# Optimization experiments

Measured on AMD Instinct MI355X. Metric: run time of the kernel, lower is better.

## Reference

```python
import jax, jax.numpy as jnp
import numpy as np

N = 50000
E = 800000
IN = 128
HID = 320
HEADS = 4
D = HID // HEADS  # 80
EPS = 1e-5
NEG_SLOPE = 0.2


def sage_conv(x, src, dst, wl, bl, wr, n):
    # PyG SAGEConv (mean aggr): out = lin_l(mean_j x_j) + lin_r(x_i)
    msg = x[src]                                               # [E, HID]
    s = jax.ops.segment_sum(msg, dst, num_segments=n)          # [N, HID]
    cnt = jax.ops.segment_sum(jnp.ones((src.shape[0], 1), x.dtype), dst, num_segments=n)
    mean = s / jnp.maximum(cnt, 1.0)
    return mean @ wl + bl + x @ wr


def gat_conv(x, src, dst, w, a_src, a_dst, b, n):
    # PyG GATConv with add_self_loops=True, concat=True
    loop = jnp.arange(n, dtype=src.dtype)
    src = jnp.concatenate([src, loop])
    dst = jnp.concatenate([dst, loop])
    xh = (x @ w).reshape(n, HEADS, D)                          # [N, H, D]
    al = jnp.sum(xh * a_src, axis=-1)                          # [N, H] (source term)
    ar = jnp.sum(xh * a_dst, axis=-1)                          # [N, H] (target term)
    e = jax.nn.leaky_relu(al[src] + ar[dst], NEG_SLOPE)        # [E', H]
    m = jax.ops.segment_max(e, dst, num_segments=n)            # [N, H]
    m = jnp.where(jnp.isfinite(m), m, 0.0)
    ex = jnp.exp(e - m[dst])                                   # [E', H]
    den = jax.ops.segment_sum(ex, dst, num_segments=n)         # [N, H]
    num = jax.ops.segment_sum(ex[:, :, None] * xh[src], dst, num_segments=n)  # [N, H, D]
    out = num / jnp.maximum(den, 1e-16)[:, :, None]
    return out.reshape(n, HEADS * D) + b


def batch_norm(x, gamma, beta):
    # eval-mode BN with running_mean=0, running_var=1
    return x * (gamma / jnp.sqrt(1.0 + EPS)) + beta


def setup_inputs() -> dict:
    key = jax.random.key(0)
    ks = jax.random.split(key, 24)
    s = 0.05
    inp = {
        'x': jax.random.normal(ks[0], (N, IN), jnp.float32),
        'edge_index': jax.random.randint(ks[1], (2, E), 0, N, jnp.int32),
        'w_in': jax.random.normal(ks[2], (IN, HID), jnp.float32) * s,
        'b_in': jnp.zeros((HID,), jnp.float32),
        'sage0_wl': jax.random.normal(ks[3], (HID, HID), jnp.float32) * s,
        'sage0_bl': jnp.zeros((HID,), jnp.float32),
        'sage0_wr': jax.random.normal(ks[4], (HID, HID), jnp.float32) * s,
        'gat1_w': jax.random.normal(ks[5], (HID, HID), jnp.float32) * s,
        'gat1_asrc': jax.random.normal(ks[6], (HEADS, D), jnp.float32) * s,
        'gat1_adst': jax.random.normal(ks[7], (HEADS, D), jnp.float32) * s,
        'gat1_b': jnp.zeros((HID,), jnp.float32),
        'sage2_wl': jax.random.normal(ks[8], (HID, HID), jnp.float32) * s,
        'sage2_bl': jnp.zeros((HID,), jnp.float32),
        'sage2_wr': jax.random.normal(ks[9], (HID, HID), jnp.float32) * s,
        'gat3_w': jax.random.normal(ks[10], (HID, HID), jnp.float32) * s,
        'gat3_asrc': jax.random.normal(ks[11], (HEADS, D), jnp.float32) * s,
        'gat3_adst': jax.random.normal(ks[12], (HEADS, D), jnp.float32) * s,
        'gat3_b': jnp.zeros((HID,), jnp.float32),
        'bn_gamma': jnp.ones((4, HID), jnp.float32),
        'bn_beta': jnp.zeros((4, HID), jnp.float32),
        'cls_w1': jax.random.normal(ks[13], (HID, HID // 2), jnp.float32) * s,
        'cls_b1': jnp.zeros((HID // 2,), jnp.float32),
        'cls_w2': jax.random.normal(ks[14], (HID // 2, 2), jnp.float32) * s,
        'cls_b2': jnp.zeros((2,), jnp.float32),
    }
    return inp


def reference(x, edge_index, w_in, b_in,
              sage0_wl, sage0_bl, sage0_wr,
              gat1_w, gat1_asrc, gat1_adst, gat1_b,
              sage2_wl, sage2_bl, sage2_wr,
              gat3_w, gat3_asrc, gat3_adst, gat3_b,
              bn_gamma, bn_beta,
              cls_w1, cls_b1, cls_w2, cls_b2):
    src, dst = edge_index[0], edge_index[1]
    h = jax.nn.relu(x @ w_in + b_in)  # dropout is identity in eval
    # layer 0: SAGE
    h = sage_conv(h, src, dst, sage0_wl, sage0_bl, sage0_wr, N)
    h = jax.nn.relu(batch_norm(h, bn_gamma[0], bn_beta[0]))
    # layer 1: GAT
    h = gat_conv(h, src, dst, gat1_w, gat1_asrc, gat1_adst, gat1_b, N)
    h = jax.nn.relu(batch_norm(h, bn_gamma[1], bn_beta[1]))
    # layer 2: SAGE
    h = sage_conv(h, src, dst, sage2_wl, sage2_bl, sage2_wr, N)
    h = jax.nn.relu(batch_norm(h, bn_gamma[2], bn_beta[2]))
    # layer 3: GAT
    h = gat_conv(h, src, dst, gat3_w, gat3_asrc, gat3_adst, gat3_b, N)
    h = jax.nn.relu(batch_norm(h, bn_gamma[3], bn_beta[3]))
    embeddings = h
    out = jax.nn.relu(h @ cls_w1 + cls_b1) @ cls_w2 + cls_b2
    return (out, embeddings)
```

## Files before the change

kernel.cpp:

```cpp
#include <hip/hip_runtime.h>
#include <cstdint>

#define MN 50000
#define EN 800000
#define HID 320
#define HEADS 4
#define HDIM 80
#define NEG_SLOPE 0.2f

typedef __attribute__((ext_vector_type(4))) float f32x4;
typedef __attribute__((ext_vector_type(8))) short short8v;

__device__ __forceinline__ unsigned short f2bf(float f){
  unsigned u = __float_as_uint(f);
  return (unsigned short)((u + 0x7fffu + ((u >> 16) & 1u)) >> 16);
}
__device__ __forceinline__ float bf2f(unsigned short s){
  return __uint_as_float(((unsigned)s) << 16);
}
__device__ __forceinline__ void gldlds16(const void* g, void* l){
  __builtin_amdgcn_global_load_lds((const __attribute__((address_space(1))) void*)g,
                                   (__attribute__((address_space(3))) void*)l, 16, 0, 0);
}

__global__ void hist_kernel(const int* __restrict__ dst, int* __restrict__ hist, int E) {
  int e = blockIdx.x * 256 + threadIdx.x;
  if (e < E) atomicAdd(&hist[dst[e]], 1);
}

__global__ __launch_bounds__(1024) void scan_kernel(const int* __restrict__ hist,
                                                    int* __restrict__ row_off, int n) {
  __shared__ int part[1024];
  int t = threadIdx.x;
  int chunk = (n + 1023) >> 10;
  int beg = t * chunk, end = beg + chunk;
  if (end > n) end = n;
  if (beg > n) beg = n;
  int s = 0;
  for (int i = beg; i < end; i++) s += hist[i];
  part[t] = s;
  __syncthreads();
  for (int off = 1; off < 1024; off <<= 1) {
    int v = (t >= off) ? part[t - off] : 0;
    __syncthreads();
    if (t >= off) part[t] += v;
    __syncthreads();
  }
  int run = (t > 0) ? part[t - 1] : 0;
  for (int i = beg; i < end; i++) { row_off[i] = run; run += hist[i]; }
  if (t == 0) row_off[n] = part[1023];
}

__global__ void scatter_kernel(const int* __restrict__ src, const int* __restrict__ dst,
                               const int* __restrict__ row_off, int* __restrict__ cur,
                               int* __restrict__ csr_src, int E) {
  int e = blockIdx.x * 256 + threadIdx.x;
  if (e < E) {
    int d = dst[e];
    int p = atomicAdd(&cur[d], 1);
    csr_src[row_off[d] + p] = src[e];
  }
}

__global__ void wprep(const float* __restrict__ W, unsigned short* __restrict__ dst,
                      int K, int Nsz, int total) {
  int idx = blockIdx.x * 256 + threadIdx.x;
  if (idx >= total) return;
  int j = idx & 7;
  int c1 = (idx >> 3) & 3;
  int rest = idx >> 5;
  int col = rest % Nsz;
  int kt = rest / Nsz;
  int chunk = c1 ^ ((col >> 1) & 3);
  int kp = kt * 32 + chunk * 8 + j;
  int seg = kp / K;
  int k = kp - seg * K;
  float v = W[(size_t)k * Nsz + col];
  unsigned short h = f2bf(v);
  unsigned short o = (seg == 2) ? f2bf(v - bf2f(h)) : h;
  dst[(size_t)kt * Nsz * 32 + (size_t)col * 32 + c1 * 8 + j] = o;
}

template<int CW, bool SRCF32, int SEGT, int NPASS, int MODE>
__global__ __launch_bounds__(128 * CW, 4) void mfma_gemm(
    const char* __restrict__ A1, const char* __restrict__ A2,
    const char* __restrict__ Wq,
    const float* __restrict__ bias, const float* __restrict__ gamma,
    const float* __restrict__ beta, void* __restrict__ outp, int M)
{
  static_assert(!SRCF32 || CW == 4, "");
  constexpr int TPB = 128 * CW;
  constexpr int N = CW * 80;
  constexpr int NT = NPASS * 3 * SEGT;
  constexpr int TILEB = N * 64;
  constexpr int AIT = (384 + TPB - 1) / TPB;
  constexpr bool SPLITOUT = (MODE >= 2);
  constexpr bool HASBIAS = (MODE >= 1 && MODE <= 3);
  constexpr bool HASBN = (MODE == 3);
  constexpr bool HASRELU = (MODE >= 1 && MODE <= 3);
  __shared__ __align__(16) char ldsA[2 * 7680];
  __shared__ __align__(16) char ldsB[2 * TILEB];
  const int tid = threadIdx.x;
  const int lane = tid & 63;
  const int w = tid >> 6;
  const int rw = w & 1, cwv = w >> 1;
  const int bm = blockIdx.x * 96;
  const int kc = (lane >> 4) & 3;
  const int l15 = lane & 15;

  int aoff[3], boff[5];
  #pragma unroll
  for (int fr = 0; fr < 3; fr++) aoff[fr] = (rw * 48 + fr * 16 + l15) * 80 + kc * 16;
  #pragma unroll
  for (int cf = 0; cf < 5; cf++) {
    int col = cwv * 80 + cf * 16 + l15;
    boff[cf] = col * 64 + ((kc ^ ((col >> 1) & 3)) << 4);
  }

  f32x4 acc[3][5];
  #pragma unroll
  for (int i = 0; i < 3; i++)
    #pragma unroll
    for (int j = 0; j < 5; j++) { f32x4 z = {0.f, 0.f, 0.f, 0.f}; acc[i][j] = z; }

  f32x4 areg[AIT][2];
  auto issueA = [&](int t) -> bool {
    int pass = 0, tt = t;
    if constexpr (NPASS == 2) { pass = t / (3 * SEGT); tt = t - pass * (3 * SEGT); }
    int seg = tt / SEGT;
    int kk = tt - seg * SEGT;
    const char* __restrict__ base = pass ? A2 : A1;
    #pragma unroll
    for (int it = 0; it < AIT; it++) {
      int s = tid + it * TPB;
      if (s < 384) {
        int row = s >> 2, c = s & 3;
        int r = bm + row; if (r >= M) r = M - 1;
        if constexpr (SRCF32) {
          const char* p = base + (size_t)r * 512 + kk * 128 + c * 32;
          areg[it][0] = *(const f32x4*)p;
          areg[it][1] = *(const f32x4*)(p + 16);
        } else {
          const char* p = base + (size_t)r * 1280 + (seg == 1 ? 640 : 0) + kk * 64 + c * 16;
          areg[it][0] = *(const f32x4*)p;
        }
      }
    }
    return seg == 1;
  };
  auto writeA = [&](int buf, bool lo) {
    #pragma unroll
    for (int it = 0; it < AIT; it++) {
      int s = tid + it * TPB;
      if (s < 384) {
        int row = s >> 2, c = s & 3;
        char* d = &ldsA[buf * 7680 + row * 80 + c * 16];
        if constexpr (SRCF32) {
          short8v v;
          #pragma unroll
          for (int j = 0; j < 8; j++) {
            float f = (j < 4) ? areg[it][0][j] : areg[it][1][j - 4];
            unsigned short h = f2bf(f);
            unsigned short o = lo ? f2bf(f - bf2f(h)) : h;
            v[j] = (short)o;
          }
          *(short8v*)d = v;
        } else {
          f32x4 t4 = areg[it][0];
          *(short8v*)d = *(short8v*)&t4;
        }
      }
    }
  };
  auto issueB = [&](int t, int buf) {
    const char* __restrict__ src = Wq + (size_t)t * TILEB;
    for (int s = tid; s < N * 4; s += TPB)
      gldlds16(src + (size_t)s * 16, &ldsB[buf * TILEB + s * 16]);
  };

  bool plo = issueA(0);
  issueB(0, 0);
  writeA(0, plo);
  __syncthreads();

  for (int t = 0; t < NT; ++t) {
    int curb = t & 1, nxt = curb ^ 1;
    bool lo = false;
    if (t + 1 < NT) { lo = issueA(t + 1); issueB(t + 1, nxt); }
    short8v af0 = *(const short8v*)&ldsA[curb * 7680 + aoff[0]];
    short8v af1 = *(const short8v*)&ldsA[curb * 7680 + aoff[1]];
    short8v af2 = *(const short8v*)&ldsA[curb * 7680 + aoff[2]];
    #pragma unroll
    for (int cf = 0; cf < 5; cf++) {
      short8v bv = *(const short8v*)&ldsB[curb * TILEB + boff[cf]];
      acc[0][cf] = __builtin_amdgcn_mfma_f32_16x16x32_bf16(af0, bv, acc[0][cf], 0, 0, 0);
      acc[1][cf] = __builtin_amdgcn_mfma_f32_16x16x32_bf16(af1, bv, acc[1][cf], 0, 0, 0);
      acc[2][cf] = __builtin_amdgcn_mfma_f32_16x16x32_bf16(af2, bv, acc[2][cf], 0, 0, 0);
    }
    if (t + 1 < NT) writeA(nxt, lo);
    __syncthreads();
  }

  const float bnrs = 0.99999500003749971f;
  #pragma unroll
  for (int fr = 0; fr < 3; fr++) {
    int rbase = bm + rw * 48 + fr * 16 + (lane >> 4) * 4;
    #pragma unroll
    for (int cf = 0; cf < 5; cf++) {
      int col = cwv * 80 + cf * 16 + l15;
      float bi = 0.f, sc = 1.f, be = 0.f;
      if constexpr (HASBIAS) bi = bias[col];
      if constexpr (HASBN) { sc = gamma[col] * bnrs; be = beta[col]; }
      #pragma unroll
      for (int rg = 0; rg < 4; rg++) {
        int r = rbase + rg;
        if (r < M) {
          float v = acc[fr][cf][rg];
          if constexpr (HASBIAS) v += bi;
          if constexpr (HASBN) v = v * sc + be;
          if constexpr (HASRELU) v = v > 0.f ? v : 0.f;
          if constexpr (SPLITOUT) {
            unsigned short h = f2bf(v);
            unsigned short g = f2bf(v - bf2f(h));
            unsigned short* o = (unsigned short*)outp;
            o[(size_t)r * 640 + col] = h;
            o[(size_t)r * 640 + 320 + col] = g;
          } else {
            ((float*)outp)[(size_t)r * N + col] = v;
          }
        }
      }
    }
  }
}

__global__ __launch_bounds__(256) void sage_agg_split(const unsigned* __restrict__ hp,
    const int* __restrict__ row_off, const int* __restrict__ csr_src,
    unsigned* __restrict__ outp, int n) {
  int node = blockIdx.x * 8 + (threadIdx.x >> 5);
  int lane = threadIdx.x & 31;
  if (node >= n) return;
  int beg = row_off[node], end = row_off[node + 1];
  float s0[5] = {0,0,0,0,0}, s1[5] = {0,0,0,0,0};
  for (int e = beg; e < end; e++) {
    const unsigned* row = hp + (size_t)csr_src[e] * 320;
    #pragma unroll
    for (int k = 0; k < 5; k++) {
      unsigned dh = row[lane + 32 * k];
      s0[k] += bf2f((unsigned short)dh);
      s1[k] += bf2f((unsigned short)(dh >> 16));
    }
  }
  int deg = end - beg;
  float inv = 1.0f / (float)(deg > 0 ? deg : 1);
  unsigned* orow = outp + (size_t)node * 320;
  #pragma unroll
  for (int k = 0; k < 5; k++) {
    float v0 = s0[k] * inv;
    float v1 = s1[k] * inv;
    unsigned short h0 = f2bf(v0), h1 = f2bf(v1);
    unsigned short g0 = f2bf(v0 - bf2f(h0)), g1 = f2bf(v1 - bf2f(h1));
    orow[lane + 32 * k] = (unsigned)h0 | ((unsigned)h1 << 16);
    orow[160 + lane + 32 * k] = (unsigned)g0 | ((unsigned)g1 << 16);
  }
}

__global__ void gat_prep(const unsigned short* __restrict__ xs,
    const float* __restrict__ asrc, const float* __restrict__ adst,
    float* __restrict__ al, float* __restrict__ ar, int n) {
  int idx = blockIdx.x * 256 + threadIdx.x;
  if (idx >= n * HEADS) return;
  int node = idx >> 2, hh = idx & 3;
  const unsigned short* hi = xs + (size_t)node * 640 + hh * 80;
  const unsigned short* lo = hi + 320;
  const f32x4* as4 = (const f32x4*)(asrc + hh * HDIM);
  const f32x4* ad4 = (const f32x4*)(adst + hh * HDIM);
  float sl = 0.f, sr = 0.f;
  #pragma unroll
  for (int d8 = 0; d8 < 10; d8++) {
    short8v vh = *(const short8v*)(hi + d8 * 8);
    short8v vl = *(const short8v*)(lo + d8 * 8);
    f32x4 a0 = as4[2 * d8], a1 = as4[2 * d8 + 1];
    f32x4 b0 = ad4[2 * d8], b1 = ad4[2 * d8 + 1];
    #pragma unroll
    for (int j = 0; j < 4; j++) {
      float v = bf2f((unsigned short)vh[j]) + bf2f((unsigned short)vl[j]);
      sl += v * a0[j]; sr += v * b0[j];
    }
    #pragma unroll
    for (int j = 0; j < 4; j++) {
      float v = bf2f((unsigned short)vh[4 + j]) + bf2f((unsigned short)vl[4 + j]);
      sl += v * a1[j]; sr += v * b1[j];
    }
  }
  al[idx] = sl;
  ar[idx] = sr;
}

template<bool F32OUT>
__global__ __launch_bounds__(256) void gat_agg(const unsigned short* __restrict__ hp,
    const int* __restrict__ row_off, const int* __restrict__ csr_src,
    const float* __restrict__ al, const float* __restrict__ ar,
    const float* __restrict__ bias, const float* __restrict__ gamma,
    const float* __restrict__ beta, unsigned short* __restrict__ outS,
    float* __restrict__ outF, int n) {
  int node = (blockIdx.x << 2) + (threadIdx.x >> 6);
  int lane = threadIdx.x & 63;
  if (node >= n) return;
  int beg = row_off[node], end = row_off[node + 1];
  const int hh = lane >> 4;
  const int posb = hh * 80 + (lane & 15);

  float arv[4], sh[4];
  f32x4 a4i = *(const f32x4*)(al + (size_t)node * 4);
  #pragma unroll
  for (int h = 0; h < 4; h++) {
    arv[h] = ar[node * 4 + h];
    float v = a4i[h] + arv[h];
    sh[h] = fmaxf(v, NEG_SLOPE * v);
  }
  float den[4] = {1.f, 1.f, 1.f, 1.f};
  const unsigned short* selfrow = hp + (size_t)node * 640;
  float num[5];
  #pragma unroll
  for (int k = 0; k < 5; k++) {
    int p = posb + 16 * k;
    num[k] = bf2f(selfrow[p]) + bf2f(selfrow[320 + p]);
  }

  for (int e = beg; e < end; e++) {
    int s = __builtin_amdgcn_readfirstlane(csr_src[e]);
    f32x4 a4 = *(const f32x4*)(al + (size_t)s * 4);
    float ex[4];
    #pragma unroll
    for (int h = 0; h < 4; h++) {
      float v = a4[h] + arv[h];
      v = fmaxf(v, NEG_SLOPE * v);
      float r = __expf(v - sh[h]);
      ex[h] = r;
      den[h] += r;
    }
    float exsel = hh < 2 ? (hh == 0 ? ex[0] : ex[1]) : (hh == 2 ? ex[2] : ex[3]);
    const unsigned short* __restrict__ row = hp + (size_t)s * 640;
    #pragma unroll
    for (int k = 0; k < 5; k++) num[k] += exsel * bf2f(row[posb + 16 * k]);
  }

  float dsel = hh < 2 ? (hh == 0 ? den[0] : den[1]) : (hh == 2 ? den[2] : den[3]);
  float dinv = 1.0f / dsel;
  const float bnrs = 0.99999500003749971f;
  #pragma unroll
  for (int k = 0; k < 5; k++) {
    int p = posb + 16 * k;
    float v = num[k] * dinv + bias[p];
    v = v * (gamma[p] * bnrs) + beta[p];
    v = fmaxf(v, 0.f);
    unsigned short h2 = f2bf(v);
    outS[(size_t)node * 640 + p] = h2;
    outS[(size_t)node * 640 + 320 + p] = f2bf(v - bf2f(h2));
    if constexpr (F32OUT) outF[(size_t)node * 320 + p] = v;
  }
}

__global__ void cls2_kernel(const float* __restrict__ tbuf, const float* __restrict__ w2,
                            const float* __restrict__ b2, float* __restrict__ out, int M) {
  int r = blockIdx.x * 256 + threadIdx.x;
  if (r >= M) return;
  const f32x4* row = (const f32x4*)(tbuf + (size_t)r * 160);
  float a0 = b2[0], a1 = b2[1];
  #pragma unroll
  for (int d4 = 0; d4 < 40; d4++) {
    f32x4 v = row[d4];
    #pragma unroll
    for (int j = 0; j < 4; j++) {
      int d = d4 * 4 + j;
      a0 += v[j] * w2[2 * d];
      a1 += v[j] * w2[2 * d + 1];
    }
  }
  out[2 * r] = a0;
  out[2 * r + 1] = a1;
}

extern "C" void kernel_launch(void* const* d_in, const int* in_sizes, int n_in,
                              void* d_out, int out_size, void* d_ws, size_t ws_size,
                              hipStream_t stream) {
  const float* x    = (const float*)d_in[0];
  const int*   ei   = (const int*)d_in[1];
  const float* w_in = (const float*)d_in[2];
  const float* b_in = (const float*)d_in[3];
  const float* s0wl = (const float*)d_in[4];
  const float* s0bl = (const float*)d_in[5];
  const float* s0wr = (const float*)d_in[6];
  const float* g1w  = (const float*)d_in[7];
  const float* g1as = (const float*)d_in[8];
  const float* g1ad = (const float*)d_in[9];
  const float* g1b  = (const float*)d_in[10];
  const float* s2wl = (const float*)d_in[11];
  const float* s2bl = (const float*)d_in[12];
  const float* s2wr = (const float*)d_in[13];
  const float* g3w  = (const float*)d_in[14];
  const float* g3as = (const float*)d_in[15];
  const float* g3ad = (const float*)d_in[16];
  const float* g3b  = (const float*)d_in[17];
  const float* bng  = (const float*)d_in[18];
  const float* bnb  = (const float*)d_in[19];
  const float* cw1  = (const float*)d_in[20];
  const float* cb1  = (const float*)d_in[21];
  const float* cw2  = (const float*)d_in[22];
  const float* cb2  = (const float*)d_in[23];

  char* ws = (char*)d_ws;
  size_t off = 0;
  auto alloc = [&](size_t b) {
    void* p = (void*)(ws + off);
    off += (b + 255) & ~(size_t)255;
    return p;
  };
  const size_t SB = (size_t)MN * 1280;
  char* S0 = (char*)alloc(SB);
  char* S1 = (char*)alloc(SB);
  char* S2 = (char*)alloc(SB);
  char* WQ = (char*)alloc(4239360);
  float* al      = (float*)alloc((size_t)MN * HEADS * 4);
  float* ar      = (float*)alloc((size_t)MN * HEADS * 4);
  int*   row_off = (int*)alloc((size_t)(MN + 1) * 4);
  int*   hist    = (int*)alloc((size_t)MN * 4);
  int*   curw    = (int*)alloc((size_t)MN * 4);
  int*   csr     = (int*)alloc((size_t)EN * 4);

  float* outp = (float*)d_out;
  float* emb  = outp + (size_t)MN * 2;

  const int* srcp = ei;
  const int* dstp = ei + EN;

  hipMemsetAsync(hist, 0, MN * 4, stream);
  hipMemsetAsync(curw, 0, MN * 4, stream);
  hist_kernel<<<(EN + 255) / 256, 256, 0, stream>>>(dstp, hist, EN);
  scan_kernel<<<1, 1024, 0, stream>>>(hist, row_off, MN);
  scatter_kernel<<<(EN + 255) / 256, 256, 0, stream>>>(srcp, dstp, row_off, curw, csr, EN);

  char* wq_in = WQ + 0;
  char* wq_s0 = WQ + 245760;
  char* wq_g1 = WQ + 1474560;
  char* wq_s2 = WQ + 2088960;
  char* wq_g3 = WQ + 3317760;
  char* wq_cl = WQ + 3932160;
  int tot = 12 * 320 * 32;
  wprep<<<(tot + 255) / 256, 256, 0, stream>>>(w_in, (unsigned short*)wq_in, 128, 320, tot);
  tot = 30 * 320 * 32;
  wprep<<<(tot + 255) / 256, 256, 0, stream>>>(s0wl, (unsigned short*)wq_s0, 320, 320, tot);
  wprep<<<(tot + 255) / 256, 256, 0, stream>>>(s0wr, (unsigned short*)(wq_s0 + 614400), 320, 320, tot);
  wprep<<<(tot + 255) / 256, 256, 0, stream>>>(g1w,  (unsigned short*)wq_g1, 320, 320, tot);
  wprep<<<(tot + 255) / 256, 256, 0, stream>>>(s2wl, (unsigned short*)wq_s2, 320, 320, tot);
  wprep<<<(tot + 255) / 256, 256, 0, stream>>>(s2wr, (unsigned short*)(wq_s2 + 614400), 320, 320, tot);
  wprep<<<(tot + 255) / 256, 256, 0, stream>>>(g3w,  (unsigned short*)wq_g3, 320, 320, tot);
  tot = 30 * 160 * 32;
  wprep<<<(tot + 255) / 256, 256, 0, stream>>>(cw1, (unsigned short*)wq_cl, 320, 160, tot);

  const int gx = (MN + 95) / 96;
  const int ga = (MN + 3) / 4;
  const int gs = (MN + 7) / 8;

  mfma_gemm<4, true, 4, 1, 2><<<gx, 512, 0, stream>>>(
      (const char*)x, nullptr, wq_in, b_in, nullptr, nullptr, S0, MN);
  sage_agg_split<<<gs, 256, 0, stream>>>((const unsigned*)S0, row_off, csr, (unsigned*)S1, MN);
  mfma_gemm<4, false, 10, 2, 3><<<gx, 512, 0, stream>>>(
      S1, S0, wq_s0, s0bl, bng, bnb, S2, MN);
  mfma_gemm<4, false, 10, 1, 4><<<gx, 512, 0, stream>>>(
      S2, nullptr, wq_g1, nullptr, nullptr, nullptr, emb, MN);
  gat_prep<<<(MN * HEADS + 255) / 256, 256, 0, stream>>>(
      (const unsigned short*)emb, g1as, g1ad, al, ar, MN);
  gat_agg<false><<<ga, 256, 0, stream>>>(
      (const unsigned short*)emb, row_off, csr, al, ar, g1b, bng + 320, bnb + 320,
      (unsigned short*)S0, nullptr, MN);
  sage_agg_split<<<gs, 256, 0, stream>>>((const unsigned*)S0, row_off, csr, (unsigned*)S1, MN);
  mfma_gemm<4, false, 10, 2, 3><<<gx, 512, 0, stream>>>(
      S1, S0, wq_s2, s2bl, bng + 640, bnb + 640, S2, MN);
  mfma_gemm<4, false, 10, 1, 4><<<gx, 512, 0, stream>>>(
      S2, nullptr, wq_g3, nullptr, nullptr, nullptr, S0, MN);
  gat_prep<<<(MN * HEADS + 255) / 256, 256, 0, stream>>>(
      (const unsigned short*)S0, g3as, g3ad, al, ar, MN);
  gat_agg<true><<<ga, 256, 0, stream>>>(
      (const unsigned short*)S0, row_off, csr, al, ar, g3b, bng + 960, bnb + 960,
      (unsigned short*)S1, emb, MN);
  mfma_gemm<2, false, 10, 1, 1><<<gx, 256, 0, stream>>>(
      S1, nullptr, wq_cl, cb1, nullptr, nullptr, S2, MN);
  cls2_kernel<<<(MN + 255) / 256, 256, 0, stream>>>((const float*)S2, cw2, cb2, outp, MN);
}
```

Before: 1.269 ms.

## Load GEMM B operand directly into registers instead of LDS staging

The weight tile is no longer staged through shared memory with global_load_lds. Each wave now reads its B fragments straight from global memory into a register double buffer, and the k-loop is unrolled by two to ping-pong those buffers. The minimum-occupancy hint in the launch bounds is dropped. This removes LDS traffic and LDS footprint for B, but waves that share columns now fetch B redundantly through the cache, register pressure rises, and the unroll by two assumes an even tile count.

```diff
diff --git a/kernel.cpp b/kernel.cpp
--- a/kernel.cpp
+++ b/kernel.cpp
@@ -17,10 +17,6 @@
 }
 __device__ __forceinline__ float bf2f(unsigned short s){
   return __uint_as_float(((unsigned)s) << 16);
-}
-__device__ __forceinline__ void gldlds16(const void* g, void* l){
-  __builtin_amdgcn_global_load_lds((const __attribute__((address_space(1))) void*)g,
-                                   (__attribute__((address_space(3))) void*)l, 16, 0, 0);
 }
 
 __global__ void hist_kernel(const int* __restrict__ dst, int* __restrict__ hist, int E) {
@@ -82,7 +78,7 @@
 }
 
 template<int CW, bool SRCF32, int SEGT, int NPASS, int MODE>
-__global__ __launch_bounds__(128 * CW, 4) void mfma_gemm(
+__global__ __launch_bounds__(128 * CW) void mfma_gemm(
     const char* __restrict__ A1, const char* __restrict__ A2,
     const char* __restrict__ Wq,
     const float* __restrict__ bias, const float* __restrict__ gamma,
@@ -99,7 +95,6 @@
   constexpr bool HASBN = (MODE == 3);
   constexpr bool HASRELU = (MODE >= 1 && MODE <= 3);
   __shared__ __align__(16) char ldsA[2 * 7680];
-  __shared__ __align__(16) char ldsB[2 * TILEB];
   const int tid = threadIdx.x;
   const int lane = tid & 63;
   const int w = tid >> 6;
@@ -108,13 +103,13 @@
   const int kc = (lane >> 4) & 3;
   const int l15 = lane & 15;
 
-  int aoff[3], boff[5];
+  int aoff[3], bgoff[5];
   #pragma unroll
   for (int fr = 0; fr < 3; fr++) aoff[fr] = (rw * 48 + fr * 16 + l15) * 80 + kc * 16;
   #pragma unroll
   for (int cf = 0; cf < 5; cf++) {
     int col = cwv * 80 + cf * 16 + l15;
-    boff[cf] = col * 64 + ((kc ^ ((col >> 1) & 3)) << 4);
+    bgoff[cf] = col * 64 + ((kc ^ ((col >> 1) & 3)) << 4);
   }
 
   f32x4 acc[3][5];
@@ -172,33 +167,38 @@
       }
     }
   };
-  auto issueB = [&](int t, int buf) {
+
+  short8v bA[5], bB[5];
+  auto loadB = [&](int t, short8v (&dst)[5]) {
     const char* __restrict__ src = Wq + (size_t)t * TILEB;
-    for (int s = tid; s < N * 4; s += TPB)
-      gldlds16(src + (size_t)s * 16, &ldsB[buf * TILEB + s * 16]);
+    #pragma unroll
+    for (int cf = 0; cf < 5; cf++) dst[cf] = *(const short8v*)(src + bgoff[cf]);
   };
 
+  auto step = [&](int t, int buf, short8v (&bcur)[5], short8v (&bnxt)[5]) {
+    bool lo = false;
+    if (t + 1 < NT) { lo = issueA(t + 1); loadB(t + 1, bnxt); }
+    short8v af0 = *(const short8v*)&ldsA[buf * 7680 + aoff[0]];
+    short8v af1 = *(const short8v*)&ldsA[buf * 7680 + aoff[1]];
+    short8v af2 = *(const short8v*)&ldsA[buf * 7680 + aoff[2]];
+    #pragma unroll
+    for (int cf = 0; cf < 5; cf++) {
+      acc[0][cf] = __builtin_amdgcn_mfma_f32_16x16x32_bf16(af0, bcur[cf], acc[0][cf], 0, 0, 0);
+      acc[1][cf] = __builtin_amdgcn_mfma_f32_16x16x32_bf16(af1, bcur[cf], acc[1][cf], 0, 0, 0);
+      acc[2][cf] = __builtin_amdgcn_mfma_f32_16x16x32_bf16(af2, bcur[cf], acc[2][cf], 0, 0, 0);
+    }
+    if (t + 1 < NT) writeA(buf ^ 1, lo);
+    __syncthreads();
+  };
+
   bool plo = issueA(0);
-  issueB(0, 0);
+  loadB(0, bA);
   writeA(0, plo);
   __syncthreads();
 
-  for (int t = 0; t < NT; ++t) {
-    int curb = t & 1, nxt = curb ^ 1;
-    bool lo = false;
-    if (t + 1 < NT) { lo = issueA(t + 1); issueB(t + 1, nxt); }
-    short8v af0 = *(const short8v*)&ldsA[curb * 7680 + aoff[0]];
-    short8v af1 = *(const short8v*)&ldsA[curb * 7680 + aoff[1]];
-    short8v af2 = *(const short8v*)&ldsA[curb * 7680 + aoff[2]];
-    #pragma unroll
-    for (int cf = 0; cf < 5; cf++) {
-      short8v bv = *(const short8v*)&ldsB[curb * TILEB + boff[cf]];
-      acc[0][cf] = __builtin_amdgcn_mfma_f32_16x16x32_bf16(af0, bv, acc[0][cf], 0, 0, 0);
-      acc[1][cf] = __builtin_amdgcn_mfma_f32_16x16x32_bf16(af1, bv, acc[1][cf], 0, 0, 0);
-      acc[2][cf] = __builtin_amdgcn_mfma_f32_16x16x32_bf16(af2, bv, acc[2][cf], 0, 0, 0);
-    }
-    if (t + 1 < NT) writeA(nxt, lo);
-    __syncthreads();
+  for (int t = 0; t < NT; t += 2) {
+    step(t, 0, bA, bB);
+    step(t + 1, 1, bB, bA);
   }
 
   const float bnrs = 0.99999500003749971f;
```

Measured after the change: 1.298 ms. +2.3%, slower.
